# Kernel optimization log

Measured on AMD Instinct MI355X. Metric: run time of the kernel, lower is better.

The kernel has to match this reference:

```python
import jax, jax.numpy as jnp
import numpy as np

B, C_IN, C_OUT, C_KEY, N = 8, 512, 512, 256, 2048


def setup_inputs() -> dict:
    key = jax.random.key(0)
    k1, k2, k3, k4 = jax.random.split(key, 4)
    x = jax.random.normal(k1, (B, C_IN, N), dtype=jnp.float32)
    # Conv1d(kernel=1, bias=False) weights -> plain linear maps over channel dim
    Wq = jax.random.normal(k2, (C_KEY, C_IN), dtype=jnp.float32) * (1.0 / np.sqrt(C_IN))
    Wk = jax.random.normal(k3, (C_KEY, C_IN), dtype=jnp.float32) * (1.0 / np.sqrt(C_IN))
    Wv = jax.random.normal(k4, (C_OUT, C_IN), dtype=jnp.float32) * (1.0 / np.sqrt(C_IN))
    return {"x": x, "Wq": Wq, "Wk": Wk, "Wv": Wv}


def reference(x, Wq, Wk, Wv):
    # 1x1 conv projections: [B, C, N] -> [B, Ck/Co, N]
    q = jnp.einsum("oc,bcn->bon", Wq, x)
    k = jnp.einsum("oc,bcn->bon", Wk, x)
    v = jnpqv = jnp.einsum("oc,bcn->bon", Wv, x)
    # sim_map[b,i,j] = sum_c k[b,c,i] * q[b,c,j]  (unscaled)
    sim = jnp.einsum("bci,bcj->bij", k, q)  # [B, N, N]
    attn = jax.nn.softmax(sim, axis=-1)
    # out = value @ sim_map, then permute(0,2,1) -> [B, N, C_out]
    out = jnp.einsum("bck,bkm->bmc", jnpqv, attn)
    return out
```

## Files before the change

kernel.cpp:

```cpp
#include <hip/hip_runtime.h>

typedef _Float16 half8 __attribute__((ext_vector_type(8)));
typedef _Float16 half4v __attribute__((ext_vector_type(4)));
typedef _Float16 half2v __attribute__((ext_vector_type(2)));
typedef float f32x4 __attribute__((ext_vector_type(4)));

#define ASYNC_CP16(gp, lp)                                       \
  __builtin_amdgcn_global_load_lds(                              \
      (const __attribute__((address_space(1))) void*)(gp),       \
      (__attribute__((address_space(3))) void*)(lp), 16, 0, 0)

static __device__ __forceinline__ half8 mulw(half8 a, half8 s) {
  half8 o;
#pragma unroll
  for (int j = 0; j < 8; j++) o[j] = a[j] * s[j];
  return o;
}

__global__ __launch_bounds__(256) void conv_w(const float* __restrict__ Wq,
                                              const float* __restrict__ Wk,
                                              const float* __restrict__ Wv,
                                              _Float16* __restrict__ Wb) {
  int idx = blockIdx.x * 256 + threadIdx.x;
  int row = idx >> 9;
  float v;
  if (row < 256)      v = Wq[idx];
  else if (row < 512) v = Wk[idx - 256 * 512];
  else                v = Wv[idx - 512 * 512];
  Wb[idx] = (_Float16)v;
}

__global__ __launch_bounds__(256) void conv_xT(const float* __restrict__ x,
                                               _Float16* __restrict__ xT) {
  __shared__ float T[32][33];
  const int b = blockIdx.z;
  const int n0 = blockIdx.x * 32, c0 = blockIdx.y * 32;
  const int t = threadIdx.x;
  const float* xb = x + (size_t)b * 512 * 2048;
  const int n2 = t & 15, cr = t >> 4;
#pragma unroll
  for (int r = 0; r < 2; r++) {
    int c = cr + r * 16;
    float2 v = *(const float2*)&xb[(size_t)(c0 + c) * 2048 + n0 + n2 * 2];
    T[c][n2 * 2] = v.x;
    T[c][n2 * 2 + 1] = v.y;
  }
  __syncthreads();
  _Float16* xtb = xT + (size_t)b * 2048 * 512;
  const int c2 = t & 15, nr = t >> 4;
#pragma unroll
  for (int r = 0; r < 2; r++) {
    int n = nr + r * 16;
    half2v h;
    h[0] = (_Float16)T[c2 * 2][n];
    h[1] = (_Float16)T[c2 * 2 + 1][n];
    *(half2v*)&xtb[(size_t)(n0 + n) * 512 + c0 + c2 * 2] = h;
  }
}

template <typename OutT, int BUFS, int MODE>
__global__ __launch_bounds__(256) void gemm_nt(
    const _Float16* __restrict__ A, const _Float16* __restrict__ B,
    OutT* __restrict__ C, OutT* __restrict__ C2, int K, int lda, int ldb,
    int ldc, int ldc2, long sA, long sB, long sC, float* __restrict__ pm,
    float* __restrict__ ps) {
  A += (size_t)blockIdx.z * sA;
  B += (size_t)blockIdx.z * sB;
  C += (size_t)blockIdx.z * sC;
  if constexpr (MODE == 1) C2 += (size_t)blockIdx.z * sC;
  const int m_blk = blockIdx.y * 128, n_blk = blockIdx.x * 128;

  __shared__ __align__(16) _Float16 As[BUFS][4096];
  __shared__ __align__(16) _Float16 Bs[BUFS][4096];

  const int t = threadIdx.x;
  const int lane = t & 63, wave = t >> 6;
  const int quad = lane >> 4, l16 = lane & 15;
  const int wm = (wave & 1) * 64, wn = (wave >> 1) * 64;

  const int srow = 16 * wave + (lane >> 2);
  const int schunk = (lane & 3) ^ ((lane >> 3) & 3);
  const _Float16* gA0 = A + (size_t)(m_blk + srow) * lda + schunk * 8;
  const _Float16* gA1 = gA0 + (size_t)64 * lda;
  const _Float16* gB0 = B + (size_t)(n_blk + srow) * ldb + schunk * 8;
  const _Float16* gB1 = gB0 + (size_t)64 * ldb;
  const int lofs = wave * 512 + lane * 8;

  const int rchunk = (quad ^ ((l16 >> 1) & 3)) * 8;

  f32x4 acc[4][4] = {};

#pragma unroll
  for (int pb = 0; pb < BUFS - 1; pb++) {
    if (pb * 32 < K) {
      ASYNC_CP16(gA0 + pb * 32, &As[pb][lofs]);
      ASYNC_CP16(gA1 + pb * 32, &As[pb][lofs + 2048]);
      ASYNC_CP16(gB0 + pb * 32, &Bs[pb][lofs]);
      ASYNC_CP16(gB1 + pb * 32, &Bs[pb][lofs + 2048]);
    }
  }

  int ib = 0;
  for (int k0 = 0; k0 < K; k0 += 32) {
    if constexpr (BUFS == 3) {
      if (k0 + 32 < K)
        asm volatile("s_waitcnt vmcnt(4)\n\ts_barrier" ::: "memory");
      else
        asm volatile("s_waitcnt vmcnt(0)\n\ts_barrier" ::: "memory");
    } else {
      asm volatile("s_waitcnt vmcnt(0)\n\ts_barrier" ::: "memory");
    }
    if (k0 + (BUFS - 1) * 32 < K) {
      int nb = ib + BUFS - 1;
      if (nb >= BUFS) nb -= BUFS;
      const int ko = k0 + (BUFS - 1) * 32;
      ASYNC_CP16(gA0 + ko, &As[nb][lofs]);
      ASYNC_CP16(gA1 + ko, &As[nb][lofs + 2048]);
      ASYNC_CP16(gB0 + ko, &Bs[nb][lofs]);
      ASYNC_CP16(gB1 + ko, &Bs[nb][lofs + 2048]);
    }
    half8 af[4], bf[4];
#pragma unroll
    for (int i = 0; i < 4; i++) {
      af[i] = *(const half8*)&As[ib][(wm + i * 16 + l16) * 32 + rchunk];
      bf[i] = *(const half8*)&Bs[ib][(wn + i * 16 + l16) * 32 + rchunk];
    }
#pragma unroll
    for (int i = 0; i < 4; i++)
#pragma unroll
      for (int j = 0; j < 4; j++)
        acc[i][j] =
            __builtin_amdgcn_mfma_f32_16x16x32_f16(af[i], bf[j], acc[i][j], 0, 0, 0);
    ib++;
    if (ib == BUFS) ib = 0;
  }

  if constexpr (MODE == 2) {
#pragma unroll
    for (int j = 0; j < 4; j++) {
      const int n0 = n_blk + wn + j * 16 + l16;
      float mx = acc[0][j][0];
#pragma unroll
      for (int i = 0; i < 4; i++)
#pragma unroll
        for (int r = 0; r < 4; r++) mx = fmaxf(mx, acc[i][j][r]);
      mx = fmaxf(mx, __shfl_xor(mx, 16, 64));
      mx = fmaxf(mx, __shfl_xor(mx, 32, 64));
      float es = 0.f;
#pragma unroll
      for (int i = 0; i < 4; i++) {
        const int m0 = m_blk + wm + i * 16 + quad * 4;
#pragma unroll
        for (int r = 0; r < 4; r++) {
          _Float16 h = (_Float16)__expf(acc[i][j][r] - mx);
          C[(size_t)(m0 + r) * ldc + n0] = h;
          es += (float)h;
        }
      }
      es += __shfl_xor(es, 16, 64);
      es += __shfl_xor(es, 32, 64);
      if (quad == 0) {
        size_t o =
            ((size_t)blockIdx.z * 32 + blockIdx.y * 2 + (wave & 1)) * 2048 + n0;
        pm[o] = mx;
        ps[o] = es;
      }
    }
  } else {
#pragma unroll
    for (int i = 0; i < 4; i++) {
      const int m0 = m_blk + wm + i * 16 + quad * 4;
#pragma unroll
      for (int j = 0; j < 4; j++) {
        const int n0 = n_blk + wn + j * 16 + l16;
        if constexpr (MODE == 1) {
          if (m_blk < 512) {
            half4v h;
#pragma unroll
            for (int r = 0; r < 4; r++) h[r] = (_Float16)acc[i][j][r];
            *(half4v*)&C[(size_t)n0 * ldc + m0] = h;
          } else {
#pragma unroll
            for (int r = 0; r < 4; r++)
              C2[(size_t)(m0 - 512 + r) * ldc2 + n0] = (OutT)acc[i][j][r];
          }
        } else {
#pragma unroll
          for (int r = 0; r < 4; r++)
            C[(size_t)(m0 + r) * ldc + n0] = (OutT)acc[i][j][r];
        }
      }
    }
  }
}

__global__ __launch_bounds__(256) void colstats2(const float* __restrict__ pm,
                                                 const float* __restrict__ ps,
                                                 _Float16* __restrict__ scl) {
  const int idx = blockIdx.x * 256 + threadIdx.x;
  const int b = idx >> 11, col = idx & 2047;
  const float* pmb = pm + (size_t)b * 32 * 2048 + col;
  const float* psb = ps + (size_t)b * 32 * 2048 + col;
  float pv[32];
  float m = -3.0e38f;
#pragma unroll
  for (int i = 0; i < 32; i++) {
    pv[i] = pmb[(size_t)i * 2048];
    m = fmaxf(m, pv[i]);
  }
  float s = 0.f;
#pragma unroll
  for (int i = 0; i < 32; i++) {
    pv[i] = __expf(pv[i] - m);
    s += psb[(size_t)i * 2048] * pv[i];
  }
  const float inv = 1.0f / s;
  _Float16* so = scl + (size_t)b * 32 * 2048 + col;
#pragma unroll
  for (int i = 0; i < 32; i++) so[(size_t)i * 2048] = (_Float16)(pv[i] * inv);
}

__global__ __launch_bounds__(512) void gemm_av(const _Float16* __restrict__ P,
                                               const _Float16* __restrict__ V,
                                               const _Float16* __restrict__ scl,
                                               float* __restrict__ C,
                                               int cbatch) {
  int lin = blockIdx.x, z, idx;
  if (cbatch == 8) {
    z = lin & 7;
    idx = lin >> 3;
  } else {
    z = lin >> 5;
    idx = lin & 31;
  }
  const int n_blk = (idx & 1) * 256;
  const int m_blk = (idx >> 1) * 128;
  P += (size_t)z * 2048 * 2048;
  V += (size_t)z * 512 * 2048;
  scl += (size_t)z * 32 * 2048;
  C += (size_t)z * 2048 * 512;

  __shared__ __align__(16) _Float16 As[2][2][4096];
  __shared__ __align__(16) _Float16 Bs[2][2][8192];

  const int t = threadIdx.x;
  const int lane = t & 63, wave = t >> 6;
  const int quad = lane >> 4, l16 = lane & 15;
  const int wm = (wave & 1) * 64, wn = (wave >> 1) * 64;

  const int arow = t >> 2;
  const int aslot = t & 3;
  const int adc = aslot ^ ((arow >> 1) & 3);
  const _Float16* gA = P + (size_t)(m_blk + arow) * 2048 + adc * 8;
  const _Float16* gS = scl + (size_t)((m_blk + arow) >> 6) * 2048 + adc * 8;
  const int awofs = arow * 32 + aslot * 8;

  const int brow0 = (wave << 4) + (lane >> 2);
  const int bdc = (lane & 3) ^ ((brow0 >> 1) & 3);
  const _Float16* gB = V + (size_t)(n_blk + brow0) * 2048 + bdc * 8;
  const int bwofs = wave << 9;

  const int rchunk = (quad ^ ((l16 >> 1) & 3)) * 8;

  f32x4 acc[4][4] = {};

  ASYNC_CP16(gB, &Bs[0][0][bwofs]);
  ASYNC_CP16(gB + (size_t)128 * 2048, &Bs[0][0][4096 + bwofs]);
  ASYNC_CP16(gB + 32, &Bs[0][1][bwofs]);
  ASYNC_CP16(gB + (size_t)128 * 2048 + 32, &Bs[0][1][4096 + bwofs]);
  {
    half8 a00 = *(const half8*)(gA);
    half8 s00 = *(const half8*)(gS);
    half8 a01 = *(const half8*)(gA + 32);
    half8 s01 = *(const half8*)(gS + 32);
    *(half8*)&As[0][0][awofs] = mulw(a00, s00);
    *(half8*)&As[0][1][awofs] = mulw(a01, s01);
  }
  half8 pA0 = *(const half8*)(gA + 64);
  half8 pS0 = *(const half8*)(gS + 64);
  half8 pA1 = *(const half8*)(gA + 96);
  half8 pS1 = *(const half8*)(gS + 96);
  asm volatile("s_waitcnt vmcnt(4) lgkmcnt(0)\n\ts_barrier" ::: "memory");
  __builtin_amdgcn_sched_barrier(0);

  for (int T = 0; T < 32; T++) {
    const int c = T & 1, n = c ^ 1;
    const int k1 = (T + 1) * 64;
    const int k2 = (T + 2) * 64;
    half8 af[4], bf[4];
#pragma unroll
    for (int i = 0; i < 4; i++) {
      af[i] = *(const half8*)&As[c][0][(wm + i * 16 + l16) * 32 + rchunk];
      bf[i] = *(const half8*)&Bs[c][0][(wn + i * 16 + l16) * 32 + rchunk];
    }
    if (T < 31) {
      ASYNC_CP16(gB + k1, &Bs[n][0][bwofs]);
      ASYNC_CP16(gB + (size_t)128 * 2048 + k1, &Bs[n][0][4096 + bwofs]);
      ASYNC_CP16(gB + k1 + 32, &Bs[n][1][bwofs]);
      ASYNC_CP16(gB + (size_t)128 * 2048 + k1 + 32, &Bs[n][1][4096 + bwofs]);
      *(half8*)&As[n][0][awofs] = mulw(pA0, pS0);
    }
    asm volatile("s_barrier" ::: "memory");
    __builtin_amdgcn_sched_barrier(0);
    __builtin_amdgcn_s_setprio(1);
#pragma unroll
    for (int i = 0; i < 4; i++)
#pragma unroll
      for (int j = 0; j < 4; j++)
        acc[i][j] =
            __builtin_amdgcn_mfma_f32_16x16x32_f16(af[i], bf[j], acc[i][j], 0, 0, 0);
    __builtin_amdgcn_s_setprio(0);
    asm volatile("s_barrier" ::: "memory");
    __builtin_amdgcn_sched_barrier(0);
    half8 af2[4], bf2[4];
#pragma unroll
    for (int i = 0; i < 4; i++) {
      af2[i] = *(const half8*)&As[c][1][(wm + i * 16 + l16) * 32 + rchunk];
      bf2[i] = *(const half8*)&Bs[c][1][(wn + i * 16 + l16) * 32 + rchunk];
    }
    half8 fA0, fS0, fA1, fS1;
    if (T < 30) {
      fA0 = *(const half8*)(gA + k2);
      fS0 = *(const half8*)(gS + k2);
      fA1 = *(const half8*)(gA + k2 + 32);
      fS1 = *(const half8*)(gS + k2 + 32);
    }
    if (T < 31) *(half8*)&As[n][1][awofs] = mulw(pA1, pS1);
    if (T < 30) {
      pA0 = fA0;
      pS0 = fS0;
      pA1 = fA1;
      pS1 = fS1;
    }
    if (T < 30)
      asm volatile("s_waitcnt vmcnt(4) lgkmcnt(0)\n\ts_barrier" ::: "memory");
    else
      asm volatile("s_waitcnt vmcnt(0) lgkmcnt(0)\n\ts_barrier" ::: "memory");
    __builtin_amdgcn_sched_barrier(0);
    __builtin_amdgcn_s_setprio(1);
#pragma unroll
    for (int i = 0; i < 4; i++)
#pragma unroll
      for (int j = 0; j < 4; j++)
        acc[i][j] =
            __builtin_amdgcn_mfma_f32_16x16x32_f16(af2[i], bf2[j], acc[i][j], 0, 0, 0);
    __builtin_amdgcn_s_setprio(0);
    asm volatile("s_barrier" ::: "memory");
    __builtin_amdgcn_sched_barrier(0);
  }

#pragma unroll
  for (int i = 0; i < 4; i++) {
    const int m0 = m_blk + wm + i * 16 + quad * 4;
#pragma unroll
    for (int j = 0; j < 4; j++) {
      const int n0 = n_blk + wn + j * 16 + l16;
#pragma unroll
      for (int r = 0; r < 4; r++) C[(size_t)(m0 + r) * 512 + n0] = acc[i][j][r];
    }
  }
}

extern "C" void kernel_launch(void* const* d_in, const int* in_sizes, int n_in,
                              void* d_out, int out_size, void* d_ws,
                              size_t ws_size, hipStream_t stream) {
  const float* x = (const float*)d_in[0];
  const float* Wq = (const float*)d_in[1];
  const float* Wk = (const float*)d_in[2];
  const float* Wv = (const float*)d_in[3];
  float* out = (float*)d_out;

  char* p = (char*)d_ws;
  auto alloc = [&](size_t bytes) -> char* {
    char* r = p;
    p += (bytes + 255) & ~(size_t)255;
    return r;
  };
  const size_t NB = 8, N = 2048, CIN = 512, CO = 512;
  _Float16* Wb = (_Float16*)alloc(1024 * 512 * sizeof(_Float16));
  _Float16* xT = (_Float16*)alloc(NB * N * CIN * sizeof(_Float16));
  _Float16* qkT = (_Float16*)alloc(NB * N * 512 * sizeof(_Float16));
  _Float16* v = (_Float16*)alloc(NB * CO * N * sizeof(_Float16));
  size_t base_used = (size_t)(p - (char*)d_ws);

  const size_t per_b =
      (size_t)N * N * 2 + 2 * 32 * N * 4 + 32 * N * 2 + 8192;
  int cb = 8;
  while (cb > 1 && base_used + (size_t)cb * per_b > ws_size) cb >>= 1;
  _Float16* simH = (_Float16*)alloc((size_t)cb * N * N * 2);
  float* pm = (float*)alloc((size_t)cb * 32 * N * 4);
  float* ps = (float*)alloc((size_t)cb * 32 * N * 4);
  _Float16* scl = (_Float16*)alloc((size_t)cb * 32 * N * 2);

  conv_w<<<dim3(1024 * 512 / 256), 256, 0, stream>>>(Wq, Wk, Wv, Wb);
  conv_xT<<<dim3(64, 16, 8), 256, 0, stream>>>(x, xT);

  gemm_nt<_Float16, 3, 1><<<dim3(16, 8, 8), 256, 0, stream>>>(
      Wb, xT, qkT, v, 512, 512, 512, 512, 2048, 0, (long)(N * CIN),
      (long)(N * 512), nullptr, nullptr);

  for (int b0 = 0; b0 < 8; b0 += cb) {
    const _Float16* qT = qkT + (size_t)b0 * N * 512;
    const _Float16* kT = qkT + (size_t)b0 * N * 512 + 256;
    gemm_nt<_Float16, 2, 2><<<dim3(16, 16, cb), 256, 0, stream>>>(
        qT, kT, simH, nullptr, 256, 512, 512, 2048, 0, (long)(N * 512),
        (long)(N * 512), (long)(N * N), pm, ps);
    colstats2<<<dim3(cb * 8), 256, 0, stream>>>(pm, ps, scl);
    gemm_av<<<dim3(32 * cb), 512, 0, stream>>>(
        simH, v + (size_t)b0 * CO * N, scl, out + (size_t)b0 * N * CO, cb);
  }
}
```

Baseline: 198.5 us.

## Rework gemm_nt into 512-thread 128x256 tiles with 64-wide triple-buffered K pipeline

The projection GEMM and the similarity GEMM move from 256-thread 128x128 tiles to 512-thread 128x256 tiles. Each iteration now consumes a 64-wide K chunk split into two halves, with a triple-buffered async-to-LDS pipeline, explicit barriers and MFMA priority boosts, mirroring the structure of gemm_av. The aim is more reuse of the A tile, fewer blocks, and better overlap of global loads with MFMA work. In exchange each block uses more LDS and gets fewer blocks per CU, and K is now a compile-time tile count.

```diff
diff --git a/kernel.cpp b/kernel.cpp
--- a/kernel.cpp
+++ b/kernel.cpp
@@ -58,81 +58,99 @@
   }
 }
 
-template <typename OutT, int BUFS, int MODE>
-__global__ __launch_bounds__(256) void gemm_nt(
+#define STAGE_NT(bb, kbase)                                   \
+  ASYNC_CP16(gA + (kbase), &As[bb][0][wofs]);                 \
+  ASYNC_CP16(gA + (kbase) + 32, &As[bb][1][wofs]);            \
+  ASYNC_CP16(gB + (kbase), &Bs[bb][0][wofs]);                 \
+  ASYNC_CP16(gB2 + (kbase), &Bs[bb][0][4096 + wofs]);         \
+  ASYNC_CP16(gB + (kbase) + 32, &Bs[bb][1][wofs]);            \
+  ASYNC_CP16(gB2 + (kbase) + 32, &Bs[bb][1][4096 + wofs]);
+
+template <int MODE, int NT>
+__global__ __launch_bounds__(512) void gemm_nt(
     const _Float16* __restrict__ A, const _Float16* __restrict__ B,
-    OutT* __restrict__ C, OutT* __restrict__ C2, int K, int lda, int ldb,
+    _Float16* __restrict__ C, _Float16* __restrict__ C2, int lda, int ldb,
     int ldc, int ldc2, long sA, long sB, long sC, float* __restrict__ pm,
     float* __restrict__ ps) {
   A += (size_t)blockIdx.z * sA;
   B += (size_t)blockIdx.z * sB;
   C += (size_t)blockIdx.z * sC;
   if constexpr (MODE == 1) C2 += (size_t)blockIdx.z * sC;
-  const int m_blk = blockIdx.y * 128, n_blk = blockIdx.x * 128;
-
-  __shared__ __align__(16) _Float16 As[BUFS][4096];
-  __shared__ __align__(16) _Float16 Bs[BUFS][4096];
+  const int m_blk = blockIdx.y * 128, n_blk = blockIdx.x * 256;
+
+  __shared__ __align__(16) _Float16 As[3][2][4096];
+  __shared__ __align__(16) _Float16 Bs[3][2][8192];
 
   const int t = threadIdx.x;
   const int lane = t & 63, wave = t >> 6;
   const int quad = lane >> 4, l16 = lane & 15;
   const int wm = (wave & 1) * 64, wn = (wave >> 1) * 64;
 
-  const int srow = 16 * wave + (lane >> 2);
-  const int schunk = (lane & 3) ^ ((lane >> 3) & 3);
-  const _Float16* gA0 = A + (size_t)(m_blk + srow) * lda + schunk * 8;
-  const _Float16* gA1 = gA0 + (size_t)64 * lda;
-  const _Float16* gB0 = B + (size_t)(n_blk + srow) * ldb + schunk * 8;
-  const _Float16* gB1 = gB0 + (size_t)64 * ldb;
-  const int lofs = wave * 512 + lane * 8;
+  const int arow = t >> 2, aslot = t & 3;
+  const int adc = aslot ^ ((arow >> 1) & 3);
+  const _Float16* gA = A + (size_t)(m_blk + arow) * lda + adc * 8;
+  const _Float16* gB = B + (size_t)(n_blk + arow) * ldb + adc * 8;
+  const _Float16* gB2 = gB + (size_t)128 * ldb;
+  const int wofs = wave * 512 + lane * 8;
 
   const int rchunk = (quad ^ ((l16 >> 1) & 3)) * 8;
 
   f32x4 acc[4][4] = {};
 
-#pragma unroll
-  for (int pb = 0; pb < BUFS - 1; pb++) {
-    if (pb * 32 < K) {
-      ASYNC_CP16(gA0 + pb * 32, &As[pb][lofs]);
-      ASYNC_CP16(gA1 + pb * 32, &As[pb][lofs + 2048]);
-      ASYNC_CP16(gB0 + pb * 32, &Bs[pb][lofs]);
-      ASYNC_CP16(gB1 + pb * 32, &Bs[pb][lofs + 2048]);
-    }
-  }
-
-  int ib = 0;
-  for (int k0 = 0; k0 < K; k0 += 32) {
-    if constexpr (BUFS == 3) {
-      if (k0 + 32 < K)
-        asm volatile("s_waitcnt vmcnt(4)\n\ts_barrier" ::: "memory");
-      else
-        asm volatile("s_waitcnt vmcnt(0)\n\ts_barrier" ::: "memory");
-    } else {
-      asm volatile("s_waitcnt vmcnt(0)\n\ts_barrier" ::: "memory");
-    }
-    if (k0 + (BUFS - 1) * 32 < K) {
-      int nb = ib + BUFS - 1;
-      if (nb >= BUFS) nb -= BUFS;
-      const int ko = k0 + (BUFS - 1) * 32;
-      ASYNC_CP16(gA0 + ko, &As[nb][lofs]);
-      ASYNC_CP16(gA1 + ko, &As[nb][lofs + 2048]);
-      ASYNC_CP16(gB0 + ko, &Bs[nb][lofs]);
-      ASYNC_CP16(gB1 + ko, &Bs[nb][lofs + 2048]);
-    }
+  STAGE_NT(0, 0);
+  STAGE_NT(1, 64);
+  asm volatile("s_waitcnt vmcnt(6)\n\ts_barrier" ::: "memory");
+  __builtin_amdgcn_sched_barrier(0);
+
+  int cbuf = 0;
+  for (int T = 0; T < NT; T++) {
+    const int kb2 = (T + 2) * 64;
     half8 af[4], bf[4];
 #pragma unroll
     for (int i = 0; i < 4; i++) {
-      af[i] = *(const half8*)&As[ib][(wm + i * 16 + l16) * 32 + rchunk];
-      bf[i] = *(const half8*)&Bs[ib][(wn + i * 16 + l16) * 32 + rchunk];
-    }
+      af[i] = *(const half8*)&As[cbuf][0][(wm + i * 16 + l16) * 32 + rchunk];
+      bf[i] = *(const half8*)&Bs[cbuf][0][(wn + i * 16 + l16) * 32 + rchunk];
+    }
+    if (T + 2 < NT) {
+      int nb = cbuf + 2;
+      if (nb >= 3) nb -= 3;
+      STAGE_NT(nb, kb2);
+    }
+    asm volatile("s_barrier" ::: "memory");
+    __builtin_amdgcn_sched_barrier(0);
+    __builtin_amdgcn_s_setprio(1);
 #pragma unroll
     for (int i = 0; i < 4; i++)
 #pragma unroll
       for (int j = 0; j < 4; j++)
         acc[i][j] =
             __builtin_amdgcn_mfma_f32_16x16x32_f16(af[i], bf[j], acc[i][j], 0, 0, 0);
-    ib++;
-    if (ib == BUFS) ib = 0;
+    __builtin_amdgcn_s_setprio(0);
+    asm volatile("s_barrier" ::: "memory");
+    __builtin_amdgcn_sched_barrier(0);
+    half8 af2[4], bf2[4];
+#pragma unroll
+    for (int i = 0; i < 4; i++) {
+      af2[i] = *(const half8*)&As[cbuf][1][(wm + i * 16 + l16) * 32 + rchunk];
+      bf2[i] = *(const half8*)&Bs[cbuf][1][(wn + i * 16 + l16) * 32 + rchunk];
+    }
+    if (T + 2 < NT)
+      asm volatile("s_waitcnt vmcnt(6)\n\ts_barrier" ::: "memory");
+    else
+      asm volatile("s_waitcnt vmcnt(0)\n\ts_barrier" ::: "memory");
+    __builtin_amdgcn_sched_barrier(0);
+    __builtin_amdgcn_s_setprio(1);
+#pragma unroll
+    for (int i = 0; i < 4; i++)
+#pragma unroll
+      for (int j = 0; j < 4; j++)
+        acc[i][j] =
+            __builtin_amdgcn_mfma_f32_16x16x32_f16(af2[i], bf2[j], acc[i][j], 0, 0, 0);
+    __builtin_amdgcn_s_setprio(0);
+    asm volatile("s_barrier" ::: "memory");
+    __builtin_amdgcn_sched_barrier(0);
+    cbuf++;
+    if (cbuf == 3) cbuf = 0;
   }
 
   if constexpr (MODE == 2) {
@@ -160,8 +178,8 @@
       es += __shfl_xor(es, 16, 64);
       es += __shfl_xor(es, 32, 64);
       if (quad == 0) {
-        size_t o =
-            ((size_t)blockIdx.z * 32 + blockIdx.y * 2 + (wave & 1)) * 2048 + n0;
+        size_t o = ((size_t)blockIdx.z * 32 + blockIdx.y * 2 + (wave & 1)) *
+                       2048 + n0;
         pm[o] = mx;
         ps[o] = es;
       }
@@ -173,21 +191,15 @@
 #pragma unroll
       for (int j = 0; j < 4; j++) {
         const int n0 = n_blk + wn + j * 16 + l16;
-        if constexpr (MODE == 1) {
-          if (m_blk < 512) {
-            half4v h;
-#pragma unroll
-            for (int r = 0; r < 4; r++) h[r] = (_Float16)acc[i][j][r];
-            *(half4v*)&C[(size_t)n0 * ldc + m0] = h;
-          } else {
-#pragma unroll
-            for (int r = 0; r < 4; r++)
-              C2[(size_t)(m0 - 512 + r) * ldc2 + n0] = (OutT)acc[i][j][r];
-          }
+        if (m_blk < 512) {
+          half4v h;
+#pragma unroll
+          for (int r = 0; r < 4; r++) h[r] = (_Float16)acc[i][j][r];
+          *(half4v*)&C[(size_t)n0 * ldc + m0] = h;
         } else {
 #pragma unroll
           for (int r = 0; r < 4; r++)
-            C[(size_t)(m0 + r) * ldc + n0] = (OutT)acc[i][j][r];
+            C2[(size_t)(m0 - 512 + r) * ldc2 + n0] = (_Float16)acc[i][j][r];
         }
       }
     }
@@ -240,8 +252,8 @@
   scl += (size_t)z * 32 * 2048;
   C += (size_t)z * 2048 * 512;
 
-  __shared__ __align__(16) _Float16 As[2][2][4096];
-  __shared__ __align__(16) _Float16 Bs[2][2][8192];
+  __shared__ __align__(16) _Float16 Asv[2][2][4096];
+  __shared__ __align__(16) _Float16 Bsv[2][2][8192];
 
   const int t = threadIdx.x;
   const int lane = t & 63, wave = t >> 6;
@@ -264,17 +276,17 @@
 
   f32x4 acc[4][4] = {};
 
-  ASYNC_CP16(gB, &Bs[0][0][bwofs]);
-  ASYNC_CP16(gB + (size_t)128 * 2048, &Bs[0][0][4096 + bwofs]);
-  ASYNC_CP16(gB + 32, &Bs[0][1][bwofs]);
-  ASYNC_CP16(gB + (size_t)128 * 2048 + 32, &Bs[0][1][4096 + bwofs]);
+  ASYNC_CP16(gB, &Bsv[0][0][bwofs]);
+  ASYNC_CP16(gB + (size_t)128 * 2048, &Bsv[0][0][4096 + bwofs]);
+  ASYNC_CP16(gB + 32, &Bsv[0][1][bwofs]);
+  ASYNC_CP16(gB + (size_t)128 * 2048 + 32, &Bsv[0][1][4096 + bwofs]);
   {
     half8 a00 = *(const half8*)(gA);
     half8 s00 = *(const half8*)(gS);
     half8 a01 = *(const half8*)(gA + 32);
     half8 s01 = *(const half8*)(gS + 32);
-    *(half8*)&As[0][0][awofs] = mulw(a00, s00);
-    *(half8*)&As[0][1][awofs] = mulw(a01, s01);
+    *(half8*)&Asv[0][0][awofs] = mulw(a00, s00);
+    *(half8*)&Asv[0][1][awofs] = mulw(a01, s01);
   }
   half8 pA0 = *(const half8*)(gA + 64);
   half8 pS0 = *(const half8*)(gS + 64);
@@ -290,15 +302,15 @@
     half8 af[4], bf[4];
 #pragma unroll
     for (int i = 0; i < 4; i++) {
-      af[i] = *(const half8*)&As[c][0][(wm + i * 16 + l16) * 32 + rchunk];
-      bf[i] = *(const half8*)&Bs[c][0][(wn + i * 16 + l16) * 32 + rchunk];
+      af[i] = *(const half8*)&Asv[c][0][(wm + i * 16 + l16) * 32 + rchunk];
+      bf[i] = *(const half8*)&Bsv[c][0][(wn + i * 16 + l16) * 32 + rchunk];
     }
     if (T < 31) {
-      ASYNC_CP16(gB + k1, &Bs[n][0][bwofs]);
-      ASYNC_CP16(gB + (size_t)128 * 2048 + k1, &Bs[n][0][4096 + bwofs]);
-      ASYNC_CP16(gB + k1 + 32, &Bs[n][1][bwofs]);
-      ASYNC_CP16(gB + (size_t)128 * 2048 + k1 + 32, &Bs[n][1][4096 + bwofs]);
-      *(half8*)&As[n][0][awofs] = mulw(pA0, pS0);
+      ASYNC_CP16(gB + k1, &Bsv[n][0][bwofs]);
+      ASYNC_CP16(gB + (size_t)128 * 2048 + k1, &Bsv[n][0][4096 + bwofs]);
+      ASYNC_CP16(gB + k1 + 32, &Bsv[n][1][bwofs]);
+      ASYNC_CP16(gB + (size_t)128 * 2048 + k1 + 32, &Bsv[n][1][4096 + bwofs]);
+      *(half8*)&Asv[n][0][awofs] = mulw(pA0, pS0);
     }
     asm volatile("s_barrier" ::: "memory");
     __builtin_amdgcn_sched_barrier(0);
@@ -315,8 +327,8 @@
     half8 af2[4], bf2[4];
 #pragma unroll
     for (int i = 0; i < 4; i++) {
-      af2[i] = *(const half8*)&As[c][1][(wm + i * 16 + l16) * 32 + rchunk];
-      bf2[i] = *(const half8*)&Bs[c][1][(wn + i * 16 + l16) * 32 + rchunk];
+      af2[i] = *(const half8*)&Asv[c][1][(wm + i * 16 + l16) * 32 + rchunk];
+      bf2[i] = *(const half8*)&Bsv[c][1][(wn + i * 16 + l16) * 32 + rchunk];
     }
     half8 fA0, fS0, fA1, fS1;
     if (T < 30) {
@@ -325,7 +337,7 @@
       fA1 = *(const half8*)(gA + k2 + 32);
       fS1 = *(const half8*)(gS + k2 + 32);
     }
-    if (T < 31) *(half8*)&As[n][1][awofs] = mulw(pA1, pS1);
+    if (T < 31) *(half8*)&Asv[n][1][awofs] = mulw(pA1, pS1);
     if (T < 30) {
       pA0 = fA0;
       pS0 = fS0;
@@ -395,15 +407,15 @@
   conv_w<<<dim3(1024 * 512 / 256), 256, 0, stream>>>(Wq, Wk, Wv, Wb);
   conv_xT<<<dim3(64, 16, 8), 256, 0, stream>>>(x, xT);
 
-  gemm_nt<_Float16, 3, 1><<<dim3(16, 8, 8), 256, 0, stream>>>(
-      Wb, xT, qkT, v, 512, 512, 512, 512, 2048, 0, (long)(N * CIN),
+  gemm_nt<1, 8><<<dim3(8, 8, 8), 512, 0, stream>>>(
+      Wb, xT, qkT, v, 512, 512, 512, 2048, 0, (long)(N * CIN),
       (long)(N * 512), nullptr, nullptr);
 
   for (int b0 = 0; b0 < 8; b0 += cb) {
     const _Float16* qT = qkT + (size_t)b0 * N * 512;
     const _Float16* kT = qkT + (size_t)b0 * N * 512 + 256;
-    gemm_nt<_Float16, 2, 2><<<dim3(16, 16, cb), 256, 0, stream>>>(
-        qT, kT, simH, nullptr, 256, 512, 512, 2048, 0, (long)(N * 512),
+    gemm_nt<2, 4><<<dim3(8, 16, cb), 512, 0, stream>>>(
+        qT, kT, simH, nullptr, 512, 512, 2048, 0, (long)(N * 512),
         (long)(N * 512), (long)(N * N), pm, ps);
     colstats2<<<dim3(cb * 8), 256, 0, stream>>>(pm, ps, scl);
     gemm_av<<<dim3(32 * cb), 512, 0, stream>>>(
```

New measurement: 202.9 us. 2.2% more time.
